# Optimization experiments

Hardware: AMD Instinct MI355X
Metric: run time of the kernel (lower is better)

## Reference

```python
import jax, jax.numpy as jnp
import numpy as np

NUM_HEADS = 8

def _transpose_qkv(x, h):
    # (B, L, H) -> (B*h, L, H/h), matching torch transpose_qkv
    B, L, H = x.shape
    return x.reshape(B, L, h, H // h).transpose(0, 2, 1, 3).reshape(B * h, L, H // h)

def _transpose_output(x, h, B):
    # (B*h, L, d) -> (B, L, h*d)  (intended inverse of transpose_qkv)
    _, L, d = x.shape
    return x.reshape(B, h, L, d).transpose(0, 2, 1, 3).reshape(B, L, h * d)

def setup_inputs() -> dict:
    key = jax.random.key(0)
    ks = jax.random.split(key, 7)
    B, n, m, H = 2, 512, 512, 256
    queries = jax.random.normal(ks[0], (B, n, H), dtype=jnp.float32)
    keys = jax.random.normal(ks[1], (B, m, H), dtype=jnp.float32)
    values = jax.random.normal(ks[2], (B, m, H), dtype=jnp.float32)
    # torch Linear weights: shape (out, in), y = x @ W.T
    Wq = jax.random.normal(ks[3], (H, H), dtype=jnp.float32) * 0.02
    Wk = jax.random.normal(ks[4], (H, H), dtype=jnp.float32) * 0.02
    Wv = jax.random.normal(ks[5], (H, H), dtype=jnp.float32) * 0.02
    Wo = jax.random.normal(ks[6], (H, H), dtype=jnp.float32) * 0.02
    return {"queries": queries, "keys": keys, "values": values,
            "Wq": Wq, "Wk": Wk, "Wv": Wv, "Wo": Wo}

def reference(queries, keys, values, Wq, Wk, Wv, Wo):
    h = NUM_HEADS
    B, n, H = queries.shape
    m = keys.shape[1]
    q_proj = queries @ Wq.T            # (B, n, H)
    k_proj = keys @ Wk.T               # (B, m, H)
    # --- additive (Bahdanau) attention branch ---
    feat = jnp.tanh(q_proj[:, :, None, :] + k_proj[:, None, :, :])  # (B, n, m, H)
    scores = feat @ Wv.T                                            # (B, n, m, H)
    attn_weights = jax.nn.softmax(scores, axis=-1)                  # softmax over last dim, as in source
    # --- multi-head dot-product path ---
    q = _transpose_qkv(q_proj, h)                  # (B*h, n, d)
    k = _transpose_qkv(k_proj, h)                  # (B*h, m, d)
    v = _transpose_qkv(keys @ Wv.T, h)             # note: source builds values from keys
    d = q.shape[-1]
    s = jnp.einsum('bqd,bkd->bqk', q, k) / jnp.sqrt(jnp.asarray(d, q.dtype))
    w = jax.nn.softmax(s, axis=-1)
    out = jnp.einsum('bqk,bkd->bqd', w, v)         # (B*h, n, d)
    out = _transpose_output(out, h, B)             # (B, n, H)
    return out @ Wo.T, attn_weights
```

## Files before the change

kernel.cpp:

```cpp
#include <hip/hip_runtime.h>
#include <hip/hip_bf16.h>

#define B_  2
#define N_  512
#define M_  512
#define H_  256
#define NH_ 8
#define DH_ 32

typedef __attribute__((ext_vector_type(4))) float f32x4;
typedef __attribute__((ext_vector_type(8))) short bf16x8;

static __device__ __forceinline__ float fast_exp2(float x) { return __builtin_amdgcn_exp2f(x); }
static __device__ __forceinline__ float fast_rcp(float x)  { return __builtin_amdgcn_rcpf(x); }

static __device__ __forceinline__ unsigned short f2b(float f) {
    unsigned int u = __float_as_uint(f);
    u += 0x7fffu + ((u >> 16) & 1u);
    return (unsigned short)(u >> 16);
}

#define SOFT_BARRIER() asm volatile("s_waitcnt lgkmcnt(0)\n\ts_barrier" ::: "memory")

#define TM 8
__global__ __launch_bounds__(256) void proj3_kernel(const float* __restrict__ Q,
                                                    const float* __restrict__ K,
                                                    const float* __restrict__ Wq,
                                                    const float* __restrict__ Wk,
                                                    const float* __restrict__ Wv,
                                                    float* __restrict__ qp,
                                                    float* __restrict__ kp,
                                                    float* __restrict__ vv) {
    const int which = blockIdx.y;
    const float* X = (which == 0) ? Q : K;
    const float* W = (which == 0) ? Wq : (which == 1) ? Wk : Wv;
    float* Y = (which == 0) ? qp : (which == 1) ? kp : vv;

    __shared__ __align__(16) float xs[TM][H_];
    const int t = threadIdx.x;
    const int r0 = blockIdx.x * TM;
    for (int idx = t; idx < TM * H_; idx += 256)
        xs[idx >> 8][idx & 255] = X[(size_t)(r0 + (idx >> 8)) * H_ + (idx & 255)];
    __syncthreads();

    float acc[TM];
#pragma unroll
    for (int r = 0; r < TM; ++r) acc[r] = 0.f;

    const float* wrow = W + (size_t)t * H_;
    for (int k = 0; k < H_; k += 4) {
        float4 w4 = *(const float4*)(wrow + k);
#pragma unroll
        for (int r = 0; r < TM; ++r) {
            acc[r] += w4.x * xs[r][k] + w4.y * xs[r][k + 1] +
                      w4.z * xs[r][k + 2] + w4.w * xs[r][k + 3];
        }
    }
#pragma unroll
    for (int r = 0; r < TM; ++r) Y[(size_t)(r0 + r) * H_ + t] = acc[r];
}

__global__ __launch_bounds__(256) void proj_kernel(const float* __restrict__ X,
                                                   const float* __restrict__ W,
                                                   float* __restrict__ Y) {
    __shared__ __align__(16) float xs[TM][H_];
    const int t = threadIdx.x;
    const int r0 = blockIdx.x * TM;
    for (int idx = t; idx < TM * H_; idx += 256)
        xs[idx >> 8][idx & 255] = X[(size_t)(r0 + (idx >> 8)) * H_ + (idx & 255)];
    __syncthreads();

    float acc[TM];
#pragma unroll
    for (int r = 0; r < TM; ++r) acc[r] = 0.f;

    const float* wrow = W + (size_t)t * H_;
    for (int k = 0; k < H_; k += 4) {
        float4 w4 = *(const float4*)(wrow + k);
#pragma unroll
        for (int r = 0; r < TM; ++r) {
            acc[r] += w4.x * xs[r][k] + w4.y * xs[r][k + 1] +
                      w4.z * xs[r][k + 2] + w4.w * xs[r][k + 3];
        }
    }
#pragma unroll
    for (int r = 0; r < TM; ++r) Y[(size_t)(r0 + r) * H_ + t] = acc[r];
}

__global__ __launch_bounds__(256) void mh_attn_kernel(const float* __restrict__ qp,
                                                      const float* __restrict__ kp,
                                                      const float* __restrict__ vv,
                                                      float* __restrict__ ctx) {
    __shared__ __align__(16) float ks[128][36];
    __shared__ __align__(16) float vs[128][36];
    const int t = threadIdx.x;
    const int bh = blockIdx.x;
    const int b = bh >> 3, head = bh & 7;
    const int i0 = blockIdx.y * 32;
    const int r = t >> 3, sub = t & 7;
    const int i = i0 + r;
    const float rs = 0.17677669529663687f;
    const float C = 1.4426950408889634f;

    const float* qptr = qp + ((size_t)(b * N_ + i)) * H_ + head * DH_;
    float4 q[8];
#pragma unroll
    for (int d = 0; d < 8; ++d) q[d] = *(const float4*)(qptr + d * 4);

    float mrun = -1e30f, lrun = 0.f;
    float4 o[8];
#pragma unroll
    for (int d = 0; d < 8; ++d) o[d] = make_float4(0.f, 0.f, 0.f, 0.f);

    for (int jt = 0; jt < 4; ++jt) {
        __syncthreads();
#pragma unroll
        for (int cc = 0; cc < 4; ++cc) {
            int cIdx = t + cc * 256;
            int jr = cIdx >> 3, d4 = cIdx & 7;
            size_t gofs = ((size_t)(b * M_ + jt * 128 + jr)) * H_ + head * DH_ + d4 * 4;
            *(float4*)(&ks[jr][d4 * 4]) = *(const float4*)(kp + gofs);
            *(float4*)(&vs[jr][d4 * 4]) = *(const float4*)(vv + gofs);
        }
        __syncthreads();

        float s16[16];
#pragma unroll
        for (int jj = 0; jj < 16; ++jj) {
            const float* kr = ks[sub + jj * 8];
            float a = 0.f;
#pragma unroll
            for (int d = 0; d < 8; ++d) {
                float4 kv = *(const float4*)(kr + d * 4);
                a += q[d].x * kv.x + q[d].y * kv.y + q[d].z * kv.z + q[d].w * kv.w;
            }
            s16[jj] = a * rs;
        }
        float tm = s16[0];
#pragma unroll
        for (int jj = 1; jj < 16; ++jj) tm = fmaxf(tm, s16[jj]);
        float mnew = fmaxf(mrun, tm);
        float corr = fast_exp2((mrun - mnew) * C);
        lrun *= corr;
#pragma unroll
        for (int d = 0; d < 8; ++d) {
            o[d].x *= corr; o[d].y *= corr; o[d].z *= corr; o[d].w *= corr;
        }
        mrun = mnew;
#pragma unroll
        for (int jj = 0; jj < 16; ++jj) {
            float p = fast_exp2((s16[jj] - mrun) * C);
            lrun += p;
            const float* vr = vs[sub + jj * 8];
#pragma unroll
            for (int d = 0; d < 8; ++d) {
                float4 vx = *(const float4*)(vr + d * 4);
                o[d].x = __builtin_fmaf(p, vx.x, o[d].x);
                o[d].y = __builtin_fmaf(p, vx.y, o[d].y);
                o[d].z = __builtin_fmaf(p, vx.z, o[d].z);
                o[d].w = __builtin_fmaf(p, vx.w, o[d].w);
            }
        }
    }

#pragma unroll
    for (int mask = 1; mask < 8; mask <<= 1) {
        float om = __shfl_xor(mrun, mask, 64);
        float ol = __shfl_xor(lrun, mask, 64);
        float Mx = fmaxf(mrun, om);
        float fa = fast_exp2((mrun - Mx) * C);
        float fb = fast_exp2((om - Mx) * C);
        lrun = lrun * fa + ol * fb;
#pragma unroll
        for (int d = 0; d < 8; ++d) {
            float ox = __shfl_xor(o[d].x, mask, 64);
            float oy = __shfl_xor(o[d].y, mask, 64);
            float oz = __shfl_xor(o[d].z, mask, 64);
            float ow = __shfl_xor(o[d].w, mask, 64);
            o[d].x = o[d].x * fa + ox * fb;
            o[d].y = o[d].y * fa + oy * fb;
            o[d].z = o[d].z * fa + oz * fb;
            o[d].w = o[d].w * fa + ow * fb;
        }
        mrun = Mx;
    }
    float inv = fast_rcp(lrun);
    float4 r4 = make_float4(0.f, 0.f, 0.f, 0.f);
#pragma unroll
    for (int d = 0; d < 8; ++d) if (sub == d) r4 = o[d];
    r4.x *= inv; r4.y *= inv; r4.z *= inv; r4.w *= inv;
    *(float4*)(ctx + ((size_t)(b * N_ + i)) * H_ + head * DH_ + sub * 4) = r4;
}

#define BM2 256
#define TILES_TOTAL 2048
#define K2_BLOCKS 256

__global__ __launch_bounds__(512, 2) void addattn_kernel(const float* __restrict__ qp,
                                                         const float* __restrict__ kp,
                                                         const float* __restrict__ Wv,
                                                         float* __restrict__ attn) {
    __shared__ __align__(16) unsigned short wv_s[H_ * H_];
    __shared__ __align__(16) float qrow[H_];

    const int t = threadIdx.x;
    const int lane = t & 63;
    const int w = t >> 6;
    const int li = lane & 15;
    const int kq = lane >> 4;
    const int wrow0 = w * 32;
    const float C = 1.4426950408889634f;
    const float L2E2 = 2.885390081777927f;

#pragma unroll
    for (int it = 0; it < 16; ++it) {
        int sIdx = t + it * 512;
        int o = sIdx >> 5;
        int slot = sIdx & 31;
        const float* src = Wv + (size_t)o * H_ + slot * 8;
        float4 a = *(const float4*)(src);
        float4 bq = *(const float4*)(src + 4);
        union { unsigned short us[8]; uint4 v; } pk;
        pk.us[0] = f2b(a.x);  pk.us[1] = f2b(a.y);  pk.us[2] = f2b(a.z);  pk.us[3] = f2b(a.w);
        pk.us[4] = f2b(bq.x); pk.us[5] = f2b(bq.y); pk.us[6] = f2b(bq.z); pk.us[7] = f2b(bq.w);
        int dslot = slot ^ (o & 15);
        *(uint4*)(wv_s + (size_t)o * 256 + dslot * 8) = pk.v;
    }

    int tile = blockIdx.x;

    float4 cur[2][2];
    {
        const int b = tile >> 10;
        const int j0 = (tile & 1) * BM2;
#pragma unroll
        for (int rf = 0; rf < 2; ++rf) {
            const int jl = wrow0 + rf * 16 + li;
            const float* kr = kp + ((size_t)(b * M_ + j0 + jl)) * H_ + kq * 8;
            cur[rf][0] = *(const float4*)(kr);
            cur[rf][1] = *(const float4*)(kr + 4);
        }
    }

    for (; tile < TILES_TOTAL; tile += K2_BLOCKS) {
        const int b = tile >> 10;
        const int i = (tile >> 1) & (N_ - 1);
        const int j0 = (tile & 1) * BM2;

        SOFT_BARRIER();
        if (t < 64) *(float4*)(qrow + t * 4) = *(const float4*)(qp + ((size_t)(b * N_ + i)) * H_ + t * 4);
        SOFT_BARRIER();

        f32x4 acc[2][16];
#pragma unroll
        for (int rf = 0; rf < 2; ++rf)
#pragma unroll
            for (int c = 0; c < 16; ++c) acc[rf][c] = (f32x4){0.f, 0.f, 0.f, 0.f};

#pragma unroll
        for (int kk = 0; kk < 8; ++kk) {
            float4 nxt[2][2];
            if (kk < 7) {
#pragma unroll
                for (int rf = 0; rf < 2; ++rf) {
                    const int jl = wrow0 + rf * 16 + li;
                    const float* kr = kp + ((size_t)(b * M_ + j0 + jl)) * H_ + (kk + 1) * 32 + kq * 8;
                    nxt[rf][0] = *(const float4*)(kr);
                    nxt[rf][1] = *(const float4*)(kr + 4);
                }
            }
            float4 q0 = *(const float4*)(qrow + kk * 32 + kq * 8);
            float4 q1 = *(const float4*)(qrow + kk * 32 + kq * 8 + 4);

            bf16x8 afr[2];
#pragma unroll
            for (int rf = 0; rf < 2; ++rf) {
                float xin[8] = {cur[rf][0].x + q0.x, cur[rf][0].y + q0.y,
                                cur[rf][0].z + q0.z, cur[rf][0].w + q0.w,
                                cur[rf][1].x + q1.x, cur[rf][1].y + q1.y,
                                cur[rf][1].z + q1.z, cur[rf][1].w + q1.w};
                union { unsigned short us[8]; bf16x8 v; } au;
#pragma unroll
                for (int e = 0; e < 8; ++e) {
                    float e2 = fast_exp2(xin[e] * L2E2);
                    float th = __builtin_fmaf(-2.0f, fast_rcp(e2 + 1.0f), 1.0f);
                    au.us[e] = f2b(th);
                }
                afr[rf] = au.v;
            }

#pragma unroll
            for (int c = 0; c < 16; ++c) {
                const int o = c * 16 + li;
                const int slot = (kk * 4 + kq) ^ (o & 15);
                bf16x8 bfr = *(const bf16x8*)(wv_s + (size_t)o * 256 + slot * 8);
                acc[0][c] = __builtin_amdgcn_mfma_f32_16x16x32_bf16(afr[0], bfr, acc[0][c], 0, 0, 0);
                acc[1][c] = __builtin_amdgcn_mfma_f32_16x16x32_bf16(afr[1], bfr, acc[1][c], 0, 0, 0);
            }
            if (kk < 7) {
#pragma unroll
                for (int rf = 0; rf < 2; ++rf) { cur[rf][0] = nxt[rf][0]; cur[rf][1] = nxt[rf][1]; }
            }
        }

        if (tile + K2_BLOCKS < TILES_TOTAL) {
            const int nt = tile + K2_BLOCKS;
            const int nb = nt >> 10;
            const int nj0 = (nt & 1) * BM2;
#pragma unroll
            for (int rf = 0; rf < 2; ++rf) {
                const int jl = wrow0 + rf * 16 + li;
                const float* kr = kp + ((size_t)(nb * M_ + nj0 + jl)) * H_ + kq * 8;
                cur[rf][0] = *(const float4*)(kr);
                cur[rf][1] = *(const float4*)(kr + 4);
            }
        }

        const size_t prow = (size_t)tile * BM2;
#pragma unroll
        for (int rf = 0; rf < 2; ++rf) {
#pragma unroll
            for (int v = 0; v < 4; ++v) {
                float p[16];
                float rsum = 0.f;
#pragma unroll
                for (int c = 0; c < 16; ++c) {
                    p[c] = fast_exp2(acc[rf][c][v] * C);
                    rsum += p[c];
                }
#pragma unroll
                for (int mask = 1; mask < 16; mask <<= 1)
                    rsum += __shfl_xor(rsum, mask, 64);
                const float inv = fast_rcp(rsum);
                const int jl = wrow0 + rf * 16 + kq * 4 + v;
                float* dst = attn + (prow + jl) * (size_t)H_ + li;
#pragma unroll
                for (int c = 0; c < 16; ++c)
                    __builtin_nontemporal_store(p[c] * inv, dst + c * 16);
            }
        }
    }
}

extern "C" void kernel_launch(void* const* d_in, const int* in_sizes, int n_in,
                              void* d_out, int out_size, void* d_ws, size_t ws_size,
                              hipStream_t stream) {
    (void)in_sizes; (void)n_in; (void)out_size; (void)ws_size;
    const float* queries = (const float*)d_in[0];
    const float* keys    = (const float*)d_in[1];
    const float* Wq = (const float*)d_in[3];
    const float* Wk = (const float*)d_in[4];
    const float* Wv = (const float*)d_in[5];
    const float* Wo = (const float*)d_in[6];

    float* out0 = (float*)d_out;
    float* attn = (float*)d_out + (size_t)B_ * N_ * H_;

    float* ws  = (float*)d_ws;
    float* qp  = ws;
    float* kp  = ws + 262144;
    float* vv  = ws + 524288;
    float* ctx = ws + 786432;

    proj3_kernel<<<dim3(128, 3), dim3(256), 0, stream>>>(queries, keys, Wq, Wk, Wv, qp, kp, vv);
    mh_attn_kernel<<<dim3(16, 16), dim3(256), 0, stream>>>(qp, kp, vv, ctx);
    proj_kernel<<<dim3(128), dim3(256), 0, stream>>>(ctx, Wo, out0);
    addattn_kernel<<<dim3(K2_BLOCKS), dim3(512), 0, stream>>>(qp, kp, Wv, attn);
}
```

Before: 221.3 us.

## Store projected keys as bf16 and prefetch full next-tile key rows and query

```diff
diff --git a/kernel.cpp b/kernel.cpp
--- a/kernel.cpp
+++ b/kernel.cpp
@@ -30,7 +30,8 @@
                                                     const float* __restrict__ Wv,
                                                     float* __restrict__ qp,
                                                     float* __restrict__ kp,
-                                                    float* __restrict__ vv) {
+                                                    float* __restrict__ vv,
+                                                    unsigned short* __restrict__ kpb) {
     const int which = blockIdx.y;
     const float* X = (which == 0) ? Q : K;
     const float* W = (which == 0) ? Wq : (which == 1) ? Wk : Wv;
@@ -57,7 +58,10 @@
         }
     }
 #pragma unroll
-    for (int r = 0; r < TM; ++r) Y[(size_t)(r0 + r) * H_ + t] = acc[r];
+    for (int r = 0; r < TM; ++r) {
+        Y[(size_t)(r0 + r) * H_ + t] = acc[r];
+        if (which == 1) kpb[(size_t)(r0 + r) * H_ + t] = f2b(acc[r]);
+    }
 }
 
 __global__ __launch_bounds__(256) void proj_kernel(const float* __restrict__ X,
@@ -197,7 +201,7 @@
 #define K2_BLOCKS 256
 
 __global__ __launch_bounds__(512, 2) void addattn_kernel(const float* __restrict__ qp,
-                                                         const float* __restrict__ kp,
+                                                         const unsigned short* __restrict__ kpb,
                                                          const float* __restrict__ Wv,
                                                          float* __restrict__ attn) {
     __shared__ __align__(16) unsigned short wv_s[H_ * H_];
@@ -229,26 +233,26 @@
 
     int tile = blockIdx.x;
 
-    float4 cur[2][2];
+    uint4 kpre[2][8];
+    f32x4 qnext = (f32x4){0.f, 0.f, 0.f, 0.f};
+
     {
-        const int b = tile >> 10;
-        const int j0 = (tile & 1) * BM2;
-#pragma unroll
-        for (int rf = 0; rf < 2; ++rf) {
-            const int jl = wrow0 + rf * 16 + li;
-            const float* kr = kp + ((size_t)(b * M_ + j0 + jl)) * H_ + kq * 8;
-            cur[rf][0] = *(const float4*)(kr);
-            cur[rf][1] = *(const float4*)(kr + 4);
-        }
-    }
-
-    for (; tile < TILES_TOTAL; tile += K2_BLOCKS) {
         const int b = tile >> 10;
         const int i = (tile >> 1) & (N_ - 1);
         const int j0 = (tile & 1) * BM2;
-
+#pragma unroll
+        for (int rf = 0; rf < 2; ++rf) {
+            const unsigned short* kr = kpb + (size_t)(b * M_ + j0 + wrow0 + rf * 16 + li) * H_ + kq * 8;
+#pragma unroll
+            for (int kk = 0; kk < 8; ++kk)
+                kpre[rf][kk] = *(const uint4*)(kr + kk * 32);
+        }
+        if (t < 64) qnext = *(const f32x4*)(qp + ((size_t)(b * N_ + i)) * H_ + t * 4);
+    }
+
+    for (; tile < TILES_TOTAL; tile += K2_BLOCKS) {
         SOFT_BARRIER();
-        if (t < 64) *(float4*)(qrow + t * 4) = *(const float4*)(qp + ((size_t)(b * N_ + i)) * H_ + t * 4);
+        if (t < 64) *(f32x4*)(qrow + t * 4) = qnext;
         SOFT_BARRIER();
 
         f32x4 acc[2][16];
@@ -259,26 +263,22 @@
 
 #pragma unroll
         for (int kk = 0; kk < 8; ++kk) {
-            float4 nxt[2][2];
-            if (kk < 7) {
-#pragma unroll
-                for (int rf = 0; rf < 2; ++rf) {
-                    const int jl = wrow0 + rf * 16 + li;
-                    const float* kr = kp + ((size_t)(b * M_ + j0 + jl)) * H_ + (kk + 1) * 32 + kq * 8;
-                    nxt[rf][0] = *(const float4*)(kr);
-                    nxt[rf][1] = *(const float4*)(kr + 4);
-                }
-            }
-            float4 q0 = *(const float4*)(qrow + kk * 32 + kq * 8);
-            float4 q1 = *(const float4*)(qrow + kk * 32 + kq * 8 + 4);
+            f32x4 qs0 = *(const f32x4*)(qrow + kk * 32 + kq * 8);
+            f32x4 qs1 = *(const f32x4*)(qrow + kk * 32 + kq * 8 + 4);
 
             bf16x8 afr[2];
 #pragma unroll
             for (int rf = 0; rf < 2; ++rf) {
-                float xin[8] = {cur[rf][0].x + q0.x, cur[rf][0].y + q0.y,
-                                cur[rf][0].z + q0.z, cur[rf][0].w + q0.w,
-                                cur[rf][1].x + q1.x, cur[rf][1].y + q1.y,
-                                cur[rf][1].z + q1.z, cur[rf][1].w + q1.w};
+                const uint4 kv = kpre[rf][kk];
+                float xin[8];
+                xin[0] = __uint_as_float(kv.x << 16)          + qs0[0];
+                xin[1] = __uint_as_float(kv.x & 0xffff0000u)  + qs0[1];
+                xin[2] = __uint_as_float(kv.y << 16)          + qs0[2];
+                xin[3] = __uint_as_float(kv.y & 0xffff0000u)  + qs0[3];
+                xin[4] = __uint_as_float(kv.z << 16)          + qs1[0];
+                xin[5] = __uint_as_float(kv.z & 0xffff0000u)  + qs1[1];
+                xin[6] = __uint_as_float(kv.w << 16)          + qs1[2];
+                xin[7] = __uint_as_float(kv.w & 0xffff0000u)  + qs1[3];
                 union { unsigned short us[8]; bf16x8 v; } au;
 #pragma unroll
                 for (int e = 0; e < 8; ++e) {
@@ -297,24 +297,23 @@
                 acc[0][c] = __builtin_amdgcn_mfma_f32_16x16x32_bf16(afr[0], bfr, acc[0][c], 0, 0, 0);
                 acc[1][c] = __builtin_amdgcn_mfma_f32_16x16x32_bf16(afr[1], bfr, acc[1][c], 0, 0, 0);
             }
-            if (kk < 7) {
-#pragma unroll
-                for (int rf = 0; rf < 2; ++rf) { cur[rf][0] = nxt[rf][0]; cur[rf][1] = nxt[rf][1]; }
-            }
         }
 
         if (tile + K2_BLOCKS < TILES_TOTAL) {
             const int nt = tile + K2_BLOCKS;
             const int nb = nt >> 10;
+            const int ni = (nt >> 1) & (N_ - 1);
             const int nj0 = (nt & 1) * BM2;
 #pragma unroll
             for (int rf = 0; rf < 2; ++rf) {
-                const int jl = wrow0 + rf * 16 + li;
-                const float* kr = kp + ((size_t)(nb * M_ + nj0 + jl)) * H_ + kq * 8;
-                cur[rf][0] = *(const float4*)(kr);
-                cur[rf][1] = *(const float4*)(kr + 4);
-            }
-        }
+                const unsigned short* kr = kpb + (size_t)(nb * M_ + nj0 + wrow0 + rf * 16 + li) * H_ + kq * 8;
+#pragma unroll
+                for (int kk = 0; kk < 8; ++kk)
+                    kpre[rf][kk] = *(const uint4*)(kr + kk * 32);
+            }
+            if (t < 64) qnext = *(const f32x4*)(qp + ((size_t)(nb * N_ + ni)) * H_ + t * 4);
+        }
+        __builtin_amdgcn_sched_barrier(0);
 
         const size_t prow = (size_t)tile * BM2;
 #pragma unroll
@@ -361,9 +360,10 @@
     float* kp  = ws + 262144;
     float* vv  = ws + 524288;
     float* ctx = ws + 786432;
-
-    proj3_kernel<<<dim3(128, 3), dim3(256), 0, stream>>>(queries, keys, Wq, Wk, Wv, qp, kp, vv);
+    unsigned short* kpb = (unsigned short*)(ws + 1048576);
+
+    proj3_kernel<<<dim3(128, 3), dim3(256), 0, stream>>>(queries, keys, Wq, Wk, Wv, qp, kp, vv, kpb);
     mh_attn_kernel<<<dim3(16, 16), dim3(256), 0, stream>>>(qp, kp, vv, ctx);
     proj_kernel<<<dim3(128), dim3(256), 0, stream>>>(ctx, Wo, out0);
-    addattn_kernel<<<dim3(K2_BLOCKS), dim3(512), 0, stream>>>(qp, kp, Wv, attn);
-}
+    addattn_kernel<<<dim3(K2_BLOCKS), dim3(512), 0, stream>>>(qp, kpb, Wv, attn);
+}
```

New measurement: 240.9 us. 8.9% more time.
